# Performance work log

Measured on AMD Instinct MI355X. Metric: run time of the kernel, lower is better.

Reference implementation:

```python
import jax, jax.numpy as jnp
import numpy as np

N_NODES = 100000
N_EDGES = 3200000
N_GRAPHS = 1000


def gcn_conv(x, row, col, norm, W, b, num_nodes):
    # x: [N, F_in] -> [N, F_out]; PyG GCNConv: linear, then normalized scatter-add
    h = x @ W                                   # [N, F_out]
    msg = norm[:, None] * h[row]                # gather from source nodes
    out = jax.ops.segment_sum(msg, col, num_segments=num_nodes)  # scatter to targets
    return out + b


def gcn_norm(edge_index, edge_weight, num_nodes):
    # add self-loops with weight 1.0 (PyG default, improved=False)
    loops = jnp.arange(num_nodes, dtype=edge_index.dtype)
    row = jnp.concatenate([edge_index[0], loops])
    col = jnp.concatenate([edge_index[1], loops])
    w = jnp.concatenate([edge_weight, jnp.ones(num_nodes, edge_weight.dtype)])
    deg = jax.ops.segment_sum(w, col, num_segments=num_nodes)
    dinv = jnp.where(deg > 0, jax.lax.rsqrt(jnp.maximum(deg, 1e-30)), 0.0)
    norm = dinv[row] * w * dinv[col]
    return row, col, norm


def setup_inputs() -> dict:
    key = jax.random.key(0)
    ks = jax.random.split(key, 8)
    x = jax.random.normal(ks[0], (N_NODES, 3), dtype=jnp.float32)
    edge_index = jax.random.randint(ks[1], (2, N_EDGES), 0, N_NODES, dtype=jnp.int64)
    edge_weight = jax.random.uniform(ks[2], (N_EDGES,), dtype=jnp.float32)
    batch = jnp.sort(jax.random.randint(ks[3], (N_NODES,), 0, N_GRAPHS, dtype=jnp.int64))
    W1 = jax.random.normal(ks[4], (3, 16), dtype=jnp.float32) * (1.0 / np.sqrt(3))
    b1 = jnp.zeros((16,), jnp.float32)
    W2 = jax.random.normal(ks[5], (16, 16), dtype=jnp.float32) * 0.25
    b2 = jnp.zeros((16,), jnp.float32)
    Wlin = jax.random.normal(ks[6], (16, 7), dtype=jnp.float32) * 0.25
    blin = jnp.zeros((7,), jnp.float32)
    return {"x": x, "edge_index": edge_index, "edge_weight": edge_weight,
            "batch": batch, "W1": W1, "b1": b1, "W2": W2, "b2": b2,
            "Wlin": Wlin, "blin": blin}


def reference(x, edge_index, edge_weight, batch, W1, b1, W2, b2, Wlin, blin):
    num_nodes = x.shape[0]
    row, col, norm = gcn_norm(edge_index, edge_weight, num_nodes)
    h = jax.nn.relu(gcn_conv(x, row, col, norm, W1, b1, num_nodes))
    h = jax.nn.relu(gcn_conv(h, row, col, norm, W2, b2, num_nodes))
    pooled = jax.ops.segment_sum(h, batch, num_segments=N_GRAPHS)  # [G, 16]
    return pooled @ Wlin + blin  # [G, 7]
```

## Files before the change

### kernel.cpp

```cpp
#include <hip/hip_runtime.h>


#define SH 6
#define RB 64
#define KMAX 2048
#define KST (KMAX + 1)
#define TPB 256
#define BCAP 8192
#define PT 1024
#define PB 256
#define NP 4
#define ETCAP 12800

typedef unsigned short ushort_t;
typedef unsigned char u8;
typedef unsigned long long u64;

__device__ __forceinline__ ushort_t f2bf(float v) {
    unsigned u = __float_as_uint(v);
    u += 0x7FFFu + ((u >> 16) & 1u);
    return (ushort_t)(u >> 16);
}

__device__ __forceinline__ unsigned quantw(float w) {
    unsigned wq = (unsigned)__float2int_rn(w * 32768.0f);
    return wq > 32767u ? 32767u : wq;
}

__global__ __launch_bounds__(PT)
void k_part(const int* __restrict__ row, const int* __restrict__ col,
            const float* __restrict__ ew, unsigned* __restrict__ bcnt,
            unsigned* __restrict__ bof, uint2* __restrict__ brc,
            int E, int K, int tile, int KP) {
    __shared__ unsigned lh[KMAX];
    __shared__ unsigned cur[KMAX];
    __shared__ unsigned wt[PT / 64];
    __shared__ unsigned lc[ETCAP];
    __shared__ unsigned lp[ETCAP];
    int tid = threadIdx.x, b = blockIdx.x;
    int e0 = min(b * tile, E), e1 = min(b * tile + tile, E);
    int cnt = e1 - e0;
    unsigned base = (unsigned)e0;
    bool staged = (cnt <= ETCAP);
    for (int i = tid; i < KMAX; i += PT) lh[i] = 0u;
    __syncthreads();
    if (staged) {
        for (int j = tid; j < cnt; j += PT) {
            int e = e0 + j;
            int c = col[e];
            lc[j] = (unsigned)c;
            lp[j] = (unsigned)row[e] | (quantw(ew[e]) << 17);
            atomicAdd(&lh[c >> SH], 1u);
        }
    } else {
        for (int e = e0 + tid; e < e1; e += PT) atomicAdd(&lh[col[e] >> SH], 1u);
    }
    __syncthreads();
    for (int i = tid; i < K; i += PT) {
        unsigned c = lh[i];
        if (c) atomicAdd(&bcnt[i], c);
    }
    int i0 = tid << 1;
    unsigned a0 = lh[i0], a1 = lh[i0 + 1];
    unsigned ts = a0 + a1, v = ts;
#pragma unroll
    for (int o = 1; o < 64; o <<= 1) {
        unsigned u = __shfl_up(v, o, 64);
        if ((tid & 63) >= o) v += u;
    }
    if ((tid & 63) == 63) wt[tid >> 6] = v;
    __syncthreads();
    if (tid == 0) {
        unsigned acc = 0;
#pragma unroll
        for (int w = 0; w < PT / 64; w++) { unsigned t = wt[w]; wt[w] = acc; acc += t; }
    }
    __syncthreads();
    unsigned ex = wt[tid >> 6] + (v - ts);
    unsigned* bo = bof + (size_t)b * KST;
    cur[i0] = base + ex;          bo[i0] = base + ex;
    cur[i0 + 1] = base + ex + a0; bo[i0 + 1] = base + ex + a0;
    if (tid == PT - 1) bo[KMAX] = base + ex + ts;
    __syncthreads();
    for (int p = 0; p < NP; ++p) {
        int lo = p * KP, hi = min(lo + KP, K);
        if (staged) {
            for (int j = tid; j < cnt; j += PT) {
                unsigned c = lc[j];
                int bkt = (int)(c >> SH);
                if (bkt >= lo && bkt < hi) {
                    unsigned pos = atomicAdd(&cur[bkt], 1u);
                    brc[pos] = make_uint2(lp[j], c);
                }
            }
        } else {
            for (int e = e0 + tid; e < e1; e += PT) {
                int c = col[e];
                int bkt = c >> SH;
                if (bkt >= lo && bkt < hi) {
                    unsigned pos = atomicAdd(&cur[bkt], 1u);
                    brc[pos] = make_uint2((unsigned)row[e] | (quantw(ew[e]) << 17),
                                          (unsigned)c);
                }
            }
        }
        __syncthreads();
    }
}

__global__ void k_scan(const unsigned* __restrict__ cnt, unsigned* __restrict__ start,
                       int K) {
    __shared__ unsigned a[KMAX], b[KMAX];
    int t = threadIdx.x;
    for (int i = t; i < KMAX; i += 1024) a[i] = (i < K) ? cnt[i] : 0u;
    __syncthreads();
    unsigned *src = a, *dst = b;
    for (int off = 1; off < KMAX; off <<= 1) {
        for (int i = t; i < KMAX; i += 1024)
            dst[i] = (i >= off) ? src[i] + src[i - off] : src[i];
        __syncthreads();
        unsigned* tmp = src; src = dst; dst = tmp;
    }
    for (int i = t; i < K; i += 1024) start[i] = (i == 0) ? 0u : src[i - 1];
}

__global__ __launch_bounds__(TPB)
void k_grp(const uint2* __restrict__ brc, const unsigned* __restrict__ bof,
           const unsigned* __restrict__ bst, const float* __restrict__ x,
           const float* __restrict__ W1, unsigned* __restrict__ srt,
           unsigned* __restrict__ cptr, float* __restrict__ dinv,
           unsigned* __restrict__ g1b, float* __restrict__ acc1,
           int N, int E, int K) {
    int orig = blockIdx.x;
    int q8 = K >> 3, r8 = K & 7;
    int xcd = orig & 7, idx = orig >> 3;
    int k = (xcd < r8 ? xcd * (q8 + 1) : r8 * (q8 + 1) + (xcd - r8) * q8) + idx;
    int node0 = k << SH;

    __shared__ unsigned ebuf[BCAP];
    __shared__ u8 cbuf[BCAP];
    __shared__ u8 seg[BCAP];
    __shared__ unsigned rsrc[PB];
    __shared__ unsigned roff[PB + 1];
    __shared__ unsigned wt4[TPB / 64];
    __shared__ unsigned cnt64[RB], st64[RB], dq[RB];
    __shared__ float dl[RB], lx[RB * 3], lw[48];
    int tid = threadIdx.x;
    unsigned s = bst[k];
    if (tid < RB) { cnt64[tid] = 0u; dq[tid] = 0u; }
    if (tid < 48) lw[tid] = W1[tid];
    int nn = min(RB, N - node0);
    for (int i = tid; i < nn * 3; i += TPB) lx[i] = x[(size_t)node0 * 3 + i];

    unsigned rl;
    {
        unsigned s0 = bof[(size_t)tid * KST + k];
        unsigned s1 = bof[(size_t)tid * KST + k + 1];
        rsrc[tid] = s0;
        rl = s1 - s0;
    }
    unsigned v = rl;
#pragma unroll
    for (int o = 1; o < 64; o <<= 1) {
        unsigned u = __shfl_up(v, o, 64);
        if ((tid & 63) >= o) v += u;
    }
    if ((tid & 63) == 63) wt4[tid >> 6] = v;
    __syncthreads();
    if (tid == 0) {
        unsigned acc = 0;
#pragma unroll
        for (int w = 0; w < TPB / 64; w++) { unsigned t = wt4[w]; wt4[w] = acc; acc += t; }
    }
    __syncthreads();
    unsigned ex = wt4[tid >> 6] + (v - rl);
    roff[tid] = ex;
    if (tid == PB - 1) roff[PB] = ex + rl;
    __syncthreads();
    unsigned c = roff[PB];

    bool fits = (c <= (unsigned)BCAP);
    if (fits) {
        for (unsigned j = ex; j < ex + rl; ++j) seg[j] = (u8)tid;
        __syncthreads();
        for (unsigned j = tid; j < c; j += TPB) {
            unsigned r = seg[j];
            unsigned src = rsrc[r] + (j - roff[r]);
            uint2 p = brc[src];
            unsigned cl = p.y & 63u;
            ebuf[j] = p.x; cbuf[j] = (u8)cl;
            atomicAdd(&cnt64[cl], 1u);
            atomicAdd(&dq[cl], p.x >> 17);
        }
        __syncthreads();
        if (tid == 0) {
            unsigned acc = 0;
            for (int i = 0; i < RB; i++) { st64[i] = acc; acc += cnt64[i]; cnt64[i] = 0u; }
        }
        __syncthreads();
        for (unsigned j = tid; j < c; j += TPB) {
            unsigned cl = cbuf[j];
            unsigned pos = st64[cl] + atomicAdd(&cnt64[cl], 1u);
            srt[s + pos] = ebuf[j];
        }
    } else {
#define MAP_SRC(j, srcv)                                                       \
        {                                                                      \
            int lo = 0, hi = PB - 1;                                           \
            _Pragma("unroll")                                                  \
            for (int it = 0; it < 8; ++it) {                                   \
                int mid = (lo + hi + 1) >> 1;                                  \
                if (roff[mid] <= (j)) lo = mid; else hi = mid - 1;             \
            }                                                                  \
            (srcv) = rsrc[lo] + ((j) - roff[lo]);                              \
        }
        for (unsigned j = tid; j < c; j += TPB) {
            unsigned src; MAP_SRC(j, src);
            uint2 p = brc[src];
            unsigned cl = p.y & 63u;
            atomicAdd(&cnt64[cl], 1u);
            atomicAdd(&dq[cl], p.x >> 17);
        }
        __syncthreads();
        if (tid == 0) {
            unsigned acc = 0;
            for (int i = 0; i < RB; i++) { st64[i] = acc; acc += cnt64[i]; cnt64[i] = 0u; }
        }
        __syncthreads();
        for (unsigned j = tid; j < c; j += TPB) {
            unsigned src; MAP_SRC(j, src);
            uint2 p = brc[src];
            unsigned cl = p.y & 63u;
            unsigned pos = st64[cl] + atomicAdd(&cnt64[cl], 1u);
            srt[s + pos] = p.x;
        }
#undef MAP_SRC
    }
    __syncthreads();
    if (tid < RB) {
        float d = rsqrtf(1.0f + (float)dq[tid] * (1.0f / 32768.0f));
        dl[tid] = d;
        if (tid < nn) {
            dinv[node0 + tid] = d;
            cptr[node0 + tid] = s + st64[tid];
        }
    }
    if (tid == 0 && node0 + nn == N) cptr[N] = (unsigned)E;
    __syncthreads();
    float* gtmp = (float*)ebuf;
    for (int idx2 = tid; idx2 < nn * 16; idx2 += TPB) {
        int n = idx2 >> 4, f = idx2 & 15;
        float vv = dl[n] * (lx[n * 3] * lw[f] + lx[n * 3 + 1] * lw[16 + f] +
                            lx[n * 3 + 2] * lw[32 + f]);
        acc1[(size_t)(node0 + n) * 16 + f] = vv;
        gtmp[idx2] = vv;
    }
    __syncthreads();
    for (int idx2 = tid; idx2 < nn * 8; idx2 += TPB) {
        int n = idx2 >> 3, qq = idx2 & 7;
        g1b[(size_t)(node0 + n) * 8 + qq] =
            (unsigned)f2bf(gtmp[n * 16 + 2 * qq]) |
            ((unsigned)f2bf(gtmp[n * 16 + 2 * qq + 1]) << 16);
    }
}

__global__ __launch_bounds__(TPB)
void k_csr1(const unsigned* __restrict__ srt, const unsigned* __restrict__ cptr,
            const uint2* __restrict__ gb2, const float* __restrict__ acc1,
            const float* __restrict__ dinv, const float* __restrict__ b1,
            const float* __restrict__ W2, unsigned* __restrict__ g2b,
            float* __restrict__ acc2, int N) {
    int t = blockIdx.x * TPB + threadIdx.x;
    int c = t >> 2, f4 = t & 3;
    if (c >= N) return;
    unsigned e = cptr[c], end = cptr[c + 1];
    float s0 = 0.0f, s1 = 0.0f, s2 = 0.0f, s3 = 0.0f;
#pragma unroll 4
    for (; e < end; ++e) {
        unsigned m = srt[e];
        float w = (float)(m >> 17) * (1.0f / 32768.0f);
        uint2 u = gb2[(size_t)(m & 0x1FFFFu) * 4 + f4];
        s0 = fmaf(w, __uint_as_float(u.x << 16), s0);
        s1 = fmaf(w, __uint_as_float(u.x & 0xFFFF0000u), s1);
        s2 = fmaf(w, __uint_as_float(u.y << 16), s2);
        s3 = fmaf(w, __uint_as_float(u.y & 0xFFFF0000u), s3);
    }
    float d = dinv[c];
    const float4 se = *(const float4*)&acc1[(size_t)c * 16 + 4 * f4];
    const float4 bb = *(const float4*)&b1[4 * f4];
    float h[4];
    h[0] = fmaxf(bb.x + d * (se.x + s0), 0.0f);
    h[1] = fmaxf(bb.y + d * (se.y + s1), 0.0f);
    h[2] = fmaxf(bb.z + d * (se.z + s2), 0.0f);
    h[3] = fmaxf(bb.w + d * (se.w + s3), 0.0f);
    int base = (threadIdx.x & 63) & ~3;
    float o0 = 0.0f, o1 = 0.0f, o2 = 0.0f, o3 = 0.0f;
#pragma unroll
    for (int kk = 0; kk < 16; ++kk) {
        float hk = __shfl(h[kk & 3], base + (kk >> 2), 64);
        const float4 wv = *(const float4*)&W2[kk * 16 + 4 * f4];
        o0 = fmaf(hk, wv.x, o0);
        o1 = fmaf(hk, wv.y, o1);
        o2 = fmaf(hk, wv.z, o2);
        o3 = fmaf(hk, wv.w, o3);
    }
    float r0 = d * o0, r1 = d * o1, r2 = d * o2, r3 = d * o3;
    *(float4*)&acc2[(size_t)c * 16 + 4 * f4] = make_float4(r0, r1, r2, r3);
    g2b[(size_t)c * 8 + 2 * f4]     = (unsigned)f2bf(r0) | ((unsigned)f2bf(r1) << 16);
    g2b[(size_t)c * 8 + 2 * f4 + 1] = (unsigned)f2bf(r2) | ((unsigned)f2bf(r3) << 16);
}

__global__ __launch_bounds__(TPB)
void k_csr2(const unsigned* __restrict__ srt, const unsigned* __restrict__ cptr,
            const uint2* __restrict__ gb2, float* __restrict__ acc, int N) {
    int t = blockIdx.x * TPB + threadIdx.x;
    int c = t >> 2, f4 = t & 3;
    if (c >= N) return;
    unsigned e = cptr[c], end = cptr[c + 1];
    float s0 = 0.0f, s1 = 0.0f, s2 = 0.0f, s3 = 0.0f;
#pragma unroll 4
    for (; e < end; ++e) {
        unsigned m = srt[e];
        float w = (float)(m >> 17) * (1.0f / 32768.0f);
        uint2 u = gb2[(size_t)(m & 0x1FFFFu) * 4 + f4];
        s0 = fmaf(w, __uint_as_float(u.x << 16), s0);
        s1 = fmaf(w, __uint_as_float(u.x & 0xFFFF0000u), s1);
        s2 = fmaf(w, __uint_as_float(u.y << 16), s2);
        s3 = fmaf(w, __uint_as_float(u.y & 0xFFFF0000u), s3);
    }
    float4* p = (float4*)&acc[(size_t)c * 16 + 4 * f4];
    float4 v = *p;
    v.x += s0; v.y += s1; v.z += s2; v.w += s3;
    *p = v;
}

#define PC 1024
__global__ void k_pool(const float* __restrict__ acc2, const float* __restrict__ dinv,
                       const float* __restrict__ b2, const int* __restrict__ batch,
                       float* __restrict__ pooled, int N, int G) {
    int b0 = blockIdx.x * PC;
    int nodes = min(PC, N - b0);
    __shared__ float lacc[64 * 16];
    __shared__ int lbat[PC];
    int tid = threadIdx.x;
    for (int i = tid; i < nodes; i += 256) lbat[i] = batch[b0 + i];
    __syncthreads();
    int gmin = lbat[0], gmax = lbat[nodes - 1];
    bool fits = (gmax - gmin < 64);
    if (fits) {
        for (int i = tid; i < 64 * 16; i += 256) lacc[i] = 0.0f;
        __syncthreads();
    }
    for (int idx = tid; idx < nodes * 16; idx += 256) {
        int i = idx >> 4, f = idx & 15;
        int n = b0 + i;
        float d = dinv[n];
        float v = b2[f] + d * acc2[(size_t)n * 16 + f];
        v = v > 0.0f ? v : 0.0f;
        if (fits) atomicAdd(&lacc[(lbat[i] - gmin) * 16 + f], v);
        else      atomicAdd(&pooled[lbat[i] * 16 + f], v);
    }
    if (fits) {
        __syncthreads();
        for (int idx = tid; idx < 64 * 16; idx += 256) {
            int g = gmin + (idx >> 4);
            float v = lacc[idx];
            if (g < G && v != 0.0f) atomicAdd(&pooled[g * 16 + (idx & 15)], v);
        }
    }
}

__global__ void k_final(const float* __restrict__ pooled, const float* __restrict__ Wlin,
                        const float* __restrict__ blin, float* __restrict__ out, int G) {
    int t = blockIdx.x * blockDim.x + threadIdx.x;
    int g = t / 7, j = t % 7;
    if (g >= G) return;
    float v = blin[j];
#pragma unroll
    for (int f = 0; f < 16; f++) v += pooled[g * 16 + f] * Wlin[f * 7 + j];
    out[g * 7 + j] = v;
}

static inline int cdiv_i(long long a, long long b) { return (int)((a + b - 1) / b); }

extern "C" void kernel_launch(void* const* d_in, const int* in_sizes, int n_in,
                              void* d_out, int out_size, void* d_ws, size_t ws_size,
                              hipStream_t stream) {
    const float* x     = (const float*)d_in[0];
    const int*   ei    = (const int*)d_in[1];
    const float* ew    = (const float*)d_in[2];
    const int*   batch = (const int*)d_in[3];
    const float* W1    = (const float*)d_in[4];
    const float* b1    = (const float*)d_in[5];
    const float* W2    = (const float*)d_in[6];
    const float* b2    = (const float*)d_in[7];
    const float* Wlin  = (const float*)d_in[8];
    const float* blin  = (const float*)d_in[9];
    float* out = (float*)d_out;

    const int N = in_sizes[0] / 3;
    const int E = in_sizes[2];
    const int G = out_size / 7;
    const int K = (N + RB - 1) >> SH;
    const int tile = cdiv_i(E, PB);
    const int KP = cdiv_i(K, NP);
    const int* row = ei;
    const int* col = ei + E;

    uint2*    brc    = (uint2*)d_ws;
    unsigned* srt    = (unsigned*)(brc + E);
    float*    dinv   = (float*)(srt + E);
    unsigned* g1b    = (unsigned*)(dinv + N);
    unsigned* g2b    = g1b + (size_t)N * 8;
    float*    acc1   = (float*)(g2b + (size_t)N * 8);
    float*    acc2   = acc1 + (size_t)N * 16;
    unsigned* cptr   = (unsigned*)(acc2 + (size_t)N * 16);
    unsigned* bst    = cptr + N + 1;
    unsigned* bof    = bst + KMAX;
    unsigned* bcnt   = bof + (size_t)PB * KST;
    float*    pooled = (float*)(bcnt + KMAX);

    hipMemsetAsync(bcnt, 0, (KMAX + (size_t)G * 16) * sizeof(unsigned), stream);

    k_part<<<PB, PT, 0, stream>>>(row, col, ew, bcnt, bof, brc, E, K, tile, KP);
    k_scan<<<1, 1024, 0, stream>>>(bcnt, bst, K);
    k_grp<<<K, TPB, 0, stream>>>(brc, bof, bst, x, W1, srt, cptr, dinv, g1b, acc1,
                                 N, E, K);

    k_csr1<<<cdiv_i((long long)N * 4, TPB), TPB, 0, stream>>>(
        srt, cptr, (const uint2*)g1b, acc1, dinv, b1, W2, g2b, acc2, N);

    k_csr2<<<cdiv_i((long long)N * 4, TPB), TPB, 0, stream>>>(
        srt, cptr, (const uint2*)g2b, acc2, N);

    k_pool<<<cdiv_i(N, PC), TPB, 0, stream>>>(acc2, dinv, b2, batch, pooled, N, G);
    k_final<<<cdiv_i((long long)G * 7, TPB), TPB, 0, stream>>>(pooled, Wlin, blin, out, G);
}
```

Baseline: 250.5 us.

## Fuse bucket scan into partition kernel and pooling into second aggregation

The separate single-block scan kernel is removed. The last partition block to finish, found through an atomic done counter, now computes the bucket start offsets. The pooling kernel is folded into the layer-2 CSR aggregation, which applies bias, ReLU and the per-graph reduction in shared memory right away instead of writing acc2 back and reading it again. BCAP is also halved, which changes the shared memory footprint of k_grp. These changes drop two launches and one round trip of the node feature array, at the cost of a last-block fence pattern and more small shared-memory atomics per block.

```diff
diff --git a/kernel.cpp b/kernel.cpp
--- a/kernel.cpp
+++ b/kernel.cpp
@@ -6,11 +6,12 @@
 #define KMAX 2048
 #define KST (KMAX + 1)
 #define TPB 256
-#define BCAP 8192
+#define BCAP 4096
 #define PT 1024
 #define PB 256
 #define NP 4
 #define ETCAP 12800
+#define GSPAN 16
 
 typedef unsigned short ushort_t;
 typedef unsigned char u8;
@@ -30,11 +31,13 @@
 __global__ __launch_bounds__(PT)
 void k_part(const int* __restrict__ row, const int* __restrict__ col,
             const float* __restrict__ ew, unsigned* __restrict__ bcnt,
+            unsigned* __restrict__ done, unsigned* __restrict__ bst,
             unsigned* __restrict__ bof, uint2* __restrict__ brc,
             int E, int K, int tile, int KP) {
     __shared__ unsigned lh[KMAX];
     __shared__ unsigned cur[KMAX];
     __shared__ unsigned wt[PT / 64];
+    __shared__ unsigned lastFlag;
     __shared__ unsigned lc[ETCAP];
     __shared__ unsigned lp[ETCAP];
     int tid = threadIdx.x, b = blockIdx.x;
@@ -59,6 +62,35 @@
     for (int i = tid; i < K; i += PT) {
         unsigned c = lh[i];
         if (c) atomicAdd(&bcnt[i], c);
+    }
+    __syncthreads();
+    if (tid == 0) {
+        __threadfence();
+        lastFlag = (atomicAdd(done, 1u) == (unsigned)(gridDim.x - 1)) ? 1u : 0u;
+    }
+    __syncthreads();
+    if (lastFlag) {
+        int i0g = tid << 1;
+        unsigned g0 = (i0g < K) ? atomicAdd(&bcnt[i0g], 0u) : 0u;
+        unsigned g1 = (i0g + 1 < K) ? atomicAdd(&bcnt[i0g + 1], 0u) : 0u;
+        unsigned ts = g0 + g1, v = ts;
+#pragma unroll
+        for (int o = 1; o < 64; o <<= 1) {
+            unsigned u = __shfl_up(v, o, 64);
+            if ((tid & 63) >= o) v += u;
+        }
+        if ((tid & 63) == 63) wt[tid >> 6] = v;
+        __syncthreads();
+        if (tid == 0) {
+            unsigned acc = 0;
+#pragma unroll
+            for (int w = 0; w < PT / 64; w++) { unsigned t = wt[w]; wt[w] = acc; acc += t; }
+        }
+        __syncthreads();
+        unsigned ex = wt[tid >> 6] + (v - ts);
+        if (i0g < K) bst[i0g] = ex;
+        if (i0g + 1 < K) bst[i0g + 1] = ex + g0;
+        __syncthreads();
     }
     int i0 = tid << 1;
     unsigned a0 = lh[i0], a1 = lh[i0 + 1];
@@ -108,22 +140,6 @@
     }
 }
 
-__global__ void k_scan(const unsigned* __restrict__ cnt, unsigned* __restrict__ start,
-                       int K) {
-    __shared__ unsigned a[KMAX], b[KMAX];
-    int t = threadIdx.x;
-    for (int i = t; i < KMAX; i += 1024) a[i] = (i < K) ? cnt[i] : 0u;
-    __syncthreads();
-    unsigned *src = a, *dst = b;
-    for (int off = 1; off < KMAX; off <<= 1) {
-        for (int i = t; i < KMAX; i += 1024)
-            dst[i] = (i >= off) ? src[i] + src[i - off] : src[i];
-        __syncthreads();
-        unsigned* tmp = src; src = dst; dst = tmp;
-    }
-    for (int i = t; i < K; i += 1024) start[i] = (i == 0) ? 0u : src[i - 1];
-}
-
 __global__ __launch_bounds__(TPB)
 void k_grp(const uint2* __restrict__ brc, const unsigned* __restrict__ bof,
            const unsigned* __restrict__ bst, const float* __restrict__ x,
@@ -312,60 +328,64 @@
 
 __global__ __launch_bounds__(TPB)
 void k_csr2(const unsigned* __restrict__ srt, const unsigned* __restrict__ cptr,
-            const uint2* __restrict__ gb2, float* __restrict__ acc, int N) {
-    int t = blockIdx.x * TPB + threadIdx.x;
+            const uint2* __restrict__ gb2, const float* __restrict__ acc2,
+            const float* __restrict__ dinv, const float* __restrict__ b2,
+            const int* __restrict__ batch, float* __restrict__ pooled,
+            int N, int G) {
+    __shared__ float lacc[GSPAN * 16];
+    __shared__ int lb[64];
+    int tid = threadIdx.x;
+    int t = blockIdx.x * TPB + tid;
     int c = t >> 2, f4 = t & 3;
-    if (c >= N) return;
-    unsigned e = cptr[c], end = cptr[c + 1];
-    float s0 = 0.0f, s1 = 0.0f, s2 = 0.0f, s3 = 0.0f;
+    int c0 = blockIdx.x * 64;
+    int ncols = min(64, N - c0);
+    if (tid < ncols) lb[tid] = batch[c0 + tid];
+    if (tid < GSPAN * 16) lacc[tid] = 0.0f;
+    __syncthreads();
+    int gmin = lb[0], gmax = lb[ncols - 1];
+    bool fits = (gmax - gmin) < GSPAN;
+
+    float h0 = 0.0f, h1 = 0.0f, h2 = 0.0f, h3 = 0.0f;
+    if (c < N) {
+        unsigned e = cptr[c], end = cptr[c + 1];
+        float s0 = 0.0f, s1 = 0.0f, s2 = 0.0f, s3 = 0.0f;
 #pragma unroll 4
-    for (; e < end; ++e) {
-        unsigned m = srt[e];
-        float w = (float)(m >> 17) * (1.0f / 32768.0f);
-        uint2 u = gb2[(size_t)(m & 0x1FFFFu) * 4 + f4];
-        s0 = fmaf(w, __uint_as_float(u.x << 16), s0);
-        s1 = fmaf(w, __uint_as_float(u.x & 0xFFFF0000u), s1);
-        s2 = fmaf(w, __uint_as_float(u.y << 16), s2);
-        s3 = fmaf(w, __uint_as_float(u.y & 0xFFFF0000u), s3);
-    }
-    float4* p = (float4*)&acc[(size_t)c * 16 + 4 * f4];
-    float4 v = *p;
-    v.x += s0; v.y += s1; v.z += s2; v.w += s3;
-    *p = v;
-}
-
-#define PC 1024
-__global__ void k_pool(const float* __restrict__ acc2, const float* __restrict__ dinv,
-                       const float* __restrict__ b2, const int* __restrict__ batch,
-                       float* __restrict__ pooled, int N, int G) {
-    int b0 = blockIdx.x * PC;
-    int nodes = min(PC, N - b0);
-    __shared__ float lacc[64 * 16];
-    __shared__ int lbat[PC];
-    int tid = threadIdx.x;
-    for (int i = tid; i < nodes; i += 256) lbat[i] = batch[b0 + i];
-    __syncthreads();
-    int gmin = lbat[0], gmax = lbat[nodes - 1];
-    bool fits = (gmax - gmin < 64);
+        for (; e < end; ++e) {
+            unsigned m = srt[e];
+            float w = (float)(m >> 17) * (1.0f / 32768.0f);
+            uint2 u = gb2[(size_t)(m & 0x1FFFFu) * 4 + f4];
+            s0 = fmaf(w, __uint_as_float(u.x << 16), s0);
+            s1 = fmaf(w, __uint_as_float(u.x & 0xFFFF0000u), s1);
+            s2 = fmaf(w, __uint_as_float(u.y << 16), s2);
+            s3 = fmaf(w, __uint_as_float(u.y & 0xFFFF0000u), s3);
+        }
+        float d = dinv[c];
+        const float4 se = *(const float4*)&acc2[(size_t)c * 16 + 4 * f4];
+        const float4 bb = *(const float4*)&b2[4 * f4];
+        h0 = fmaxf(bb.x + d * (se.x + s0), 0.0f);
+        h1 = fmaxf(bb.y + d * (se.y + s1), 0.0f);
+        h2 = fmaxf(bb.z + d * (se.z + s2), 0.0f);
+        h3 = fmaxf(bb.w + d * (se.w + s3), 0.0f);
+        int g = lb[c - c0];
+        if (fits) {
+            int o = (g - gmin) * 16 + 4 * f4;
+            atomicAdd(&lacc[o],     h0);
+            atomicAdd(&lacc[o + 1], h1);
+            atomicAdd(&lacc[o + 2], h2);
+            atomicAdd(&lacc[o + 3], h3);
+        } else {
+            atomicAdd(&pooled[(size_t)g * 16 + 4 * f4],     h0);
+            atomicAdd(&pooled[(size_t)g * 16 + 4 * f4 + 1], h1);
+            atomicAdd(&pooled[(size_t)g * 16 + 4 * f4 + 2], h2);
+            atomicAdd(&pooled[(size_t)g * 16 + 4 * f4 + 3], h3);
+        }
+    }
     if (fits) {
-        for (int i = tid; i < 64 * 16; i += 256) lacc[i] = 0.0f;
-        __syncthreads();
-    }
-    for (int idx = tid; idx < nodes * 16; idx += 256) {
-        int i = idx >> 4, f = idx & 15;
-        int n = b0 + i;
-        float d = dinv[n];
-        float v = b2[f] + d * acc2[(size_t)n * 16 + f];
-        v = v > 0.0f ? v : 0.0f;
-        if (fits) atomicAdd(&lacc[(lbat[i] - gmin) * 16 + f], v);
-        else      atomicAdd(&pooled[lbat[i] * 16 + f], v);
-    }
-    if (fits) {
-        __syncthreads();
-        for (int idx = tid; idx < 64 * 16; idx += 256) {
-            int g = gmin + (idx >> 4);
-            float v = lacc[idx];
-            if (g < G && v != 0.0f) atomicAdd(&pooled[g * 16 + (idx & 15)], v);
+        __syncthreads();
+        if (tid < GSPAN * 16) {
+            int g = gmin + (tid >> 4);
+            float v = lacc[tid];
+            if (g < G && v != 0.0f) atomicAdd(&pooled[(size_t)g * 16 + (tid & 15)], v);
         }
     }
 }
@@ -418,12 +438,13 @@
     unsigned* bst    = cptr + N + 1;
     unsigned* bof    = bst + KMAX;
     unsigned* bcnt   = bof + (size_t)PB * KST;
-    float*    pooled = (float*)(bcnt + KMAX);
-
-    hipMemsetAsync(bcnt, 0, (KMAX + (size_t)G * 16) * sizeof(unsigned), stream);
-
-    k_part<<<PB, PT, 0, stream>>>(row, col, ew, bcnt, bof, brc, E, K, tile, KP);
-    k_scan<<<1, 1024, 0, stream>>>(bcnt, bst, K);
+    unsigned* done   = bcnt + KMAX;
+    float*    pooled = (float*)(done + 1);
+
+    hipMemsetAsync(bcnt, 0, (KMAX + 1 + (size_t)G * 16) * sizeof(unsigned), stream);
+
+    k_part<<<PB, PT, 0, stream>>>(row, col, ew, bcnt, done, bst, bof, brc,
+                                  E, K, tile, KP);
     k_grp<<<K, TPB, 0, stream>>>(brc, bof, bst, x, W1, srt, cptr, dinv, g1b, acc1,
                                  N, E, K);
 
@@ -431,8 +452,7 @@
         srt, cptr, (const uint2*)g1b, acc1, dinv, b1, W2, g2b, acc2, N);
 
     k_csr2<<<cdiv_i((long long)N * 4, TPB), TPB, 0, stream>>>(
-        srt, cptr, (const uint2*)g2b, acc2, N);
-
-    k_pool<<<cdiv_i(N, PC), TPB, 0, stream>>>(acc2, dinv, b2, batch, pooled, N, G);
+        srt, cptr, (const uint2*)g2b, acc2, dinv, b2, batch, pooled, N, G);
+
     k_final<<<cdiv_i((long long)G * 7, TPB), TPB, 0, stream>>>(pooled, Wlin, blin, out, G);
 }
```

Measured after the change: 221.4 us. 1.13x faster.
